# Kernel tuning notes

Hardware: AMD Instinct MI355X
Metric: run time of the kernel (lower is better)

## Reference

```python
import jax, jax.numpy as jnp
import numpy as np

DT = 0.01  # integrator base timestep (init kwarg)
DT_SCALE = 1.0


def setup_inputs() -> dict:
    key = jax.random.key(0)
    kx, kv, kf, ku, kw = jax.random.split(key, 5)
    B, D, R = 8192, 1024, 256
    scale = 1.0 / np.sqrt(D)
    return {
        "x": jax.random.normal(kx, (B, D), jnp.float32),
        "v": jax.random.normal(kv, (B, D), jnp.float32),
        "force": jax.random.normal(kf, (B, D), jnp.float32) * 0.1,
        "U": jax.random.normal(ku, (R, D), jnp.float32) * scale,
        "W": jax.random.normal(kw, (R, D), jnp.float32) * scale,
        "steps": 4,
    }


def _christoffel(v, x, U, W):
    # Low-rank Christoffel contraction Gamma(v, v; x):
    #   h = tanh(x W^T)   [B, r]  (position-dependent gating)
    #   q = v W^T         [B, r]  (velocity projection)
    #   Gamma = (h * q^2) U  [B, d]
    h = jnp.tanh(x @ W.T)
    q = v @ W.T
    return (h * q * q) @ U


def reference(x, v, force, U, W, steps):
    # topology_id == 0 (Euclidean): apply_boundary is the identity.
    dt = DT * DT_SCALE

    def dynamics(cx, cv):
        return -_christoffel(cv, cx, U, W) + force

    cx, cv = x, v
    for _ in range(steps):  # steps is a static Python int
        dx1 = cv
        dv1 = dynamics(cx, cv)
        v2 = cv + 0.5 * dt * dv1
        x2 = cx + 0.5 * dt * dx1
        dx2 = v2
        dv2 = dynamics(x2, v2)
        v3 = cv + 0.5 * dt * dv2
        x3 = cx + 0.5 * dt * dx2
        dx3 = v3
        dv3 = dynamics(x3, v3)
        v4 = cv + dt * dv3
        x4 = cx + dt * dx3
        dx4 = v4
        dv4 = dynamics(x4, v4)
        cx = cx + (dt / 6.0) * (dx1 + 2 * dx2 + 2 * dx3 + dx4)
        cv = cv + (dt / 6.0) * (dv1 + 2 * dv2 + 2 * dv3 + dv4)
    return (cx, cv)
```

## Files before the change

kernel.cpp:

```cpp
#include <hip/hip_runtime.h>


typedef __attribute__((ext_vector_type(8))) short bf16x8;
typedef __attribute__((ext_vector_type(4))) float f32x4;
typedef unsigned short us;

#define MFMA16 __builtin_amdgcn_mfma_f32_16x16x32_bf16

namespace {
constexpr int kB = 8192;
constexpr int kD = 1024;
constexpr int kR = 256;
constexpr int kBM = 16;
constexpr float kDt = 0.01f;
}

__device__ __forceinline__ us f2bf(float f) {
  union { float f; unsigned u; } w; w.f = f;
  unsigned u = w.u + (0x7FFFu + ((w.u >> 16) & 1u));
  return (us)(u >> 16);
}
__device__ __forceinline__ float ftanh(float x) {
  float e = __expf(2.f * x);
  return 1.f - 2.f / (e + 1.f);
}
__device__ __forceinline__ bf16x8 pack8(float4 a, float4 b) {
  union { bf16x8 v; us s[8]; } u;
  u.s[0] = f2bf(a.x); u.s[1] = f2bf(a.y); u.s[2] = f2bf(a.z); u.s[3] = f2bf(a.w);
  u.s[4] = f2bf(b.x); u.s[5] = f2bf(b.y); u.s[6] = f2bf(b.z); u.s[7] = f2bf(b.w);
  return u.v;
}

__global__ void prep_wu(const float* __restrict__ U, const float* __restrict__ W,
                        us* __restrict__ Wb, us* __restrict__ Ub,
                        us* __restrict__ Wf, us* __restrict__ Uf) {
  int i = blockIdx.x * blockDim.x + threadIdx.x;
  if (i < kR * kD) {
    const int r = i >> 10, k = i & 1023;
    const us wb = f2bf(W[i]), ub = f2bf(U[i]);
    Wb[i] = wb; Ub[i] = ub;
    Wf[(((size_t)(r >> 4) * 32 + (k >> 5)) << 9) +
       (((((k >> 3) & 3) << 4) | (r & 15)) << 3) + (k & 7)] = wb;
    Uf[(((size_t)(k >> 4) * 8 + (r >> 5)) << 9) +
       (((((r >> 3) & 3) << 4) | (k & 15)) << 3) + (r & 7)] = ub;
  }
}

__global__ __launch_bounds__(256) void prep_g(const us* __restrict__ Wb,
                                              const us* __restrict__ Ub,
                                              us* __restrict__ Gf) {
  const int tid = threadIdx.x;
  const int w = tid >> 6, l = tid & 63;
  const int l15 = l & 15, l4 = l >> 4;
  const int n1 = (blockIdx.x >> 3) * 32 + (w >> 1) * 16;
  const int k1 = (blockIdx.x & 7) * 32 + (w & 1) * 16;
  f32x4 acc = {0.f, 0.f, 0.f, 0.f};
  const us* wp = Wb + (size_t)(n1 + l15) * kD + l4 * 8;
  const us* up = Ub + (size_t)(k1 + l15) * kD + l4 * 8;
#pragma unroll 8
  for (int kk = 0; kk < 32; ++kk) {
    bf16x8 aw = *(const bf16x8*)(wp + kk * 32);
    bf16x8 bu = *(const bf16x8*)(up + kk * 32);
    acc = MFMA16(aw, bu, acc, 0, 0, 0);
  }
#pragma unroll
  for (int j = 0; j < 4; ++j) {
    const int n = n1 + l4 * 4 + j, k = k1 + l15;
    Gf[(((size_t)(n >> 4) * 8 + (k >> 5)) << 9) +
       (((((k >> 3) & 3) << 4) | (n & 15)) << 3) + (k & 7)] = f2bf(acc[j]);
  }
}

__global__ __launch_bounds__(1024, 4) void fused_kernel(
    const us* __restrict__ Wf, const us* __restrict__ Gf, const us* __restrict__ Uf,
    const float* __restrict__ xin, const float* __restrict__ vin,
    const float* __restrict__ force,
    float* __restrict__ cxo, float* __restrict__ cvo) {
  __shared__ __align__(16) us stg[12288];
  __shared__ __align__(16) us ct[2][kBM * kR];

  const int tid = threadIdx.x;
  const int w = tid >> 6;
  const int l = tid & 63;
  const int l15 = l & 15;
  const int l4 = l >> 4;
  const int rs = l15 & 7;
  const int brow = blockIdx.x * kBM;
  const int rn = w * 16 + l15;
  const float dt = kDt;
  const f32x4 zero4 = {0.f, 0.f, 0.f, 0.f};

  const int slotA = tid & 511;
  const int rowA = slotA >> 5, grpA = slotA & 31;
  const int soA = (rowA << 8) + ((grpA ^ (rowA & 7)) << 3);
  us* dstA = stg + ((tid >> 9) << 12);
  const float* srcA = (tid >> 9) ? vin : xin;
  const size_t gbA0 = (size_t)(brow + rowA) * kD + grpA * 8;

  f32x4 Aa = zero4, Ba = zero4, Fa = zero4;
#pragma unroll 1
  for (int ch = 0; ch < 4; ++ch) {
    const size_t gb = gbA0 + (size_t)ch * 256;
    float4 a0 = *(const float4*)(srcA + gb), a1 = *(const float4*)(srcA + gb + 4);
    float4 b0, b1;
    if (tid < 512) { b0 = *(const float4*)(force + gb); b1 = *(const float4*)(force + gb + 4); }
    if (ch) __syncthreads();
    *(bf16x8*)(dstA + soA) = pack8(a0, a1);
    if (tid < 512) *(bf16x8*)(stg + 8192 + soA) = pack8(b0, b1);
    __syncthreads();

    const us* wfp = Wf + (((size_t)(w * 32 + ch * 8)) << 9) + l * 8;
    bf16x8 bw = *(const bf16x8*)(wfp);
#pragma unroll
    for (int kk = 0; kk < 8; ++kk) {
      const bf16x8 bwc = bw;
      if (kk < 7) bw = *(const bf16x8*)(wfp + (((size_t)(kk + 1)) << 9));
      const int aoff = (l15 << 8) + (((kk * 4 + l4) ^ rs) << 3);
      bf16x8 ax = *(const bf16x8*)(stg + aoff);
      bf16x8 av = *(const bf16x8*)(stg + 4096 + aoff);
      bf16x8 af = *(const bf16x8*)(stg + 8192 + aoff);
      Aa = MFMA16(ax, bwc, Aa, 0, 0, 0);
      Ba = MFMA16(av, bwc, Ba, 0, 0, 0);
      Fa = MFMA16(af, bwc, Fa, 0, 0, 0);
    }
  }

  bf16x8 gfr[8];
  {
    const us* gfp = Gf + ((size_t)(w * 8) << 9) + l * 8;
#pragma unroll
    for (int kk = 0; kk < 8; ++kk)
      gfr[kk] = *(const bf16x8*)(gfp + ((size_t)kk << 9));
  }

  float A[4], Bv[4], Fv[4], q[4], CS[4], PS[4], Sv[4], Sx[4];
#pragma unroll
  for (int e = 0; e < 4; ++e) {
    A[e] = Aa[e]; Bv[e] = Ba[e]; Fv[e] = Fa[e]; Sv[e] = 0.f; Sx[e] = 0.f;
  }

  int wo[4];
#pragma unroll
  for (int e = 0; e < 4; ++e) {
    const int r = l4 * 4 + e;
    wo[e] = (r << 8) + ((((rn >> 3) ^ (r & 7)) << 3) | (rn & 7));
  }

  __syncthreads();
#pragma unroll 1
  for (int s = 0; s < 4; ++s) {
#pragma unroll
    for (int e = 0; e < 4; ++e) { q[e] = Bv[e]; CS[e] = 0.f; PS[e] = 0.f; }

#pragma unroll
    for (int k = 0; k < 4; ++k) {
      const float alpha = (k == 0) ? 0.f : ((k == 3) ? dt : 0.5f * dt);
      const float wk = (k == 1 || k == 2) ? 2.f : 1.f;
      const float beta = (k <= 1) ? 0.5f * dt : dt;
      float c[4];
#pragma unroll
      for (int e = 0; e < 4; ++e) {
        const float hx = A[e] + alpha * Bv[e];
        c[e] = ftanh(hx) * q[e] * q[e];
        CS[e] += wk * c[e];
      }
      if (s == 3 && k == 3) break;

      us* cb = ct[k & 1];
#pragma unroll
      for (int e = 0; e < 4; ++e) cb[wo[e]] = f2bf(c[e]);
      __syncthreads();

      f32x4 P = zero4;
#pragma unroll
      for (int kk = 0; kk < 8; ++kk) {
        bf16x8 ca = *(const bf16x8*)(cb + (l15 << 8) + (((kk * 4 + l4) ^ rs) << 3));
        P = MFMA16(ca, gfr[kk], P, 0, 0, 0);
      }
#pragma unroll
      for (int e = 0; e < 4; ++e) {
        PS[e] += wk * P[e];
        if (k < 3) q[e] = Bv[e] + beta * (Fv[e] - P[e]);
      }
    }

#pragma unroll
    for (int e = 0; e < 4; ++e) Sv[e] += CS[e];
    if (s < 3) {
      const float wsx = (float)(3 - s);
#pragma unroll
      for (int e = 0; e < 4; ++e) {
        Sx[e] += wsx * CS[e];
        A[e] += dt * Bv[e];
        Bv[e] += dt * Fv[e] - (dt / 6.f) * PS[e];
      }
    }
  }

  __syncthreads();
#pragma unroll
  for (int e = 0; e < 4; ++e) {
    ct[0][wo[e]] = f2bf(Sv[e]);
    ct[1][wo[e]] = f2bf(Sx[e]);
  }
  __syncthreads();

#pragma unroll 1
  for (int nt = 0; nt < 4; ++nt) {
    f32x4 gv = zero4, gx = zero4;
    const int d0 = w * 64 + nt * 16;
    const us* ufp = Uf + ((size_t)((w * 4 + nt) * 8) << 9) + l * 8;
#pragma unroll
    for (int kk = 0; kk < 8; ++kk) {
      const int aoff = (l15 << 8) + (((kk * 4 + l4) ^ rs) << 3);
      bf16x8 ub = *(const bf16x8*)(ufp + ((size_t)kk << 9));
      gv = MFMA16(*(const bf16x8*)(ct[0] + aoff), ub, gv, 0, 0, 0);
      gx = MFMA16(*(const bf16x8*)(ct[1] + aoff), ub, gx, 0, 0, 0);
    }
#pragma unroll
    for (int j = 0; j < 4; ++j) {
      const int row = l4 * 4 + j;
      const size_t gi = (size_t)(brow + row) * kD + d0 + l15;
      const float x0 = xin[gi], v0 = vin[gi], f = force[gi];
      cxo[gi] = x0 + 4.f * dt * v0 + 6.f * dt * dt * f - (dt * dt / 6.f) * gx[j];
      cvo[gi] = v0 + 4.f * dt * f - (dt / 6.f) * gv[j];
    }
  }
}

__global__ void copy_only_kernel(const float* __restrict__ x, const float* __restrict__ v,
                                 float* __restrict__ cx, float* __restrict__ cv) {
  const int stride = gridDim.x * blockDim.x;
  for (int i = blockIdx.x * blockDim.x + threadIdx.x; i < kB * kD; i += stride) {
    cx[i] = x[i]; cv[i] = v[i];
  }
}

extern "C" void kernel_launch(void* const* d_in, const int* in_sizes, int n_in,
                              void* d_out, int out_size, void* d_ws, size_t ws_size,
                              hipStream_t stream) {
  const float* x = (const float*)d_in[0];
  const float* v = (const float*)d_in[1];
  const float* force = (const float*)d_in[2];
  const float* U = (const float*)d_in[3];
  const float* W = (const float*)d_in[4];

  float* cx = (float*)d_out;
  float* cv = cx + (size_t)kB * kD;

  size_t off = 0;
  us* Wb = (us*)((char*)d_ws + off); off += (size_t)kR * kD * 2;
  us* Ub = (us*)((char*)d_ws + off); off += (size_t)kR * kD * 2;
  us* Wf = (us*)((char*)d_ws + off); off += (size_t)kR * kD * 2;
  us* Uf = (us*)((char*)d_ws + off); off += (size_t)kR * kD * 2;
  us* Gf = (us*)((char*)d_ws + off); off += (size_t)kR * kR * 2;

  if (ws_size < off) {
    copy_only_kernel<<<2048, 256, 0, stream>>>(x, v, cx, cv);
    return;
  }

  prep_wu<<<(kR * kD + 255) / 256, 256, 0, stream>>>(U, W, Wb, Ub, Wf, Uf);
  prep_g<<<64, 256, 0, stream>>>(Wb, Ub, Gf);
  fused_kernel<<<kB / kBM, 1024, 0, stream>>>(Wf, Gf, Uf, x, v, force, cx, cv);
}
```

Measured before the change: 117.5 us.

## Double-buffer input staging and prefetch next chunk during MFMA projection

Doubles the shared staging buffer so each of the four input chunks goes into an alternating buffer. The global loads for the next chunk are issued right after the barrier, so they overlap with the MFMA work on the current chunk, and the extra barrier before each write is removed. Every thread now loads x, v and force as float4 and packs them with the HIP bf16 intrinsics instead of hand-written rounding. The cost is a larger shared-memory footprint, which may reduce occupancy for the 1024-thread block, and one barrier before the main loop is dropped, which depends on the ct buffer not aliasing the staging area.

```diff
diff --git a/kernel.cpp b/kernel.cpp
--- a/kernel.cpp
+++ b/kernel.cpp
@@ -1,7 +1,9 @@
 #include <hip/hip_runtime.h>
+#include <hip/hip_bf16.h>
 
 
 typedef __attribute__((ext_vector_type(8))) short bf16x8;
+typedef __attribute__((ext_vector_type(4))) short bf16x4;
 typedef __attribute__((ext_vector_type(4))) float f32x4;
 typedef unsigned short us;
 
@@ -16,19 +18,19 @@
 }
 
 __device__ __forceinline__ us f2bf(float f) {
-  union { float f; unsigned u; } w; w.f = f;
-  unsigned u = w.u + (0x7FFFu + ((w.u >> 16) & 1u));
-  return (us)(u >> 16);
+  __hip_bfloat16 h = __float2bfloat16(f);
+  union { __hip_bfloat16 b; us u; } c; c.b = h;
+  return c.u;
+}
+__device__ __forceinline__ bf16x4 pack4(float4 a) {
+  union { bf16x4 v; __hip_bfloat162 h[2]; } u;
+  u.h[0] = __float22bfloat162_rn(float2{a.x, a.y});
+  u.h[1] = __float22bfloat162_rn(float2{a.z, a.w});
+  return u.v;
 }
 __device__ __forceinline__ float ftanh(float x) {
   float e = __expf(2.f * x);
   return 1.f - 2.f / (e + 1.f);
-}
-__device__ __forceinline__ bf16x8 pack8(float4 a, float4 b) {
-  union { bf16x8 v; us s[8]; } u;
-  u.s[0] = f2bf(a.x); u.s[1] = f2bf(a.y); u.s[2] = f2bf(a.z); u.s[3] = f2bf(a.w);
-  u.s[4] = f2bf(b.x); u.s[5] = f2bf(b.y); u.s[6] = f2bf(b.z); u.s[7] = f2bf(b.w);
-  return u.v;
 }
 
 __global__ void prep_wu(const float* __restrict__ U, const float* __restrict__ W,
@@ -76,7 +78,7 @@
     const float* __restrict__ xin, const float* __restrict__ vin,
     const float* __restrict__ force,
     float* __restrict__ cxo, float* __restrict__ cvo) {
-  __shared__ __align__(16) us stg[12288];
+  __shared__ __align__(16) us stg[24576];
   __shared__ __align__(16) us ct[2][kBM * kR];
 
   const int tid = threadIdx.x;
@@ -90,38 +92,43 @@
   const float dt = kDt;
   const f32x4 zero4 = {0.f, 0.f, 0.f, 0.f};
 
-  const int slotA = tid & 511;
-  const int rowA = slotA >> 5, grpA = slotA & 31;
-  const int soA = (rowA << 8) + ((grpA ^ (rowA & 7)) << 3);
-  us* dstA = stg + ((tid >> 9) << 12);
-  const float* srcA = (tid >> 9) ? vin : xin;
-  const size_t gbA0 = (size_t)(brow + rowA) * kD + grpA * 8;
+  const int prow = tid >> 6;
+  const int pg = (tid & 63) >> 1;
+  const int pso = (prow << 8) + ((pg ^ (prow & 7)) << 3) + (tid & 1) * 4;
+  const size_t pgb0 = (size_t)(brow + prow) * kD + (tid & 63) * 4;
 
   f32x4 Aa = zero4, Ba = zero4, Fa = zero4;
+  {
+    float4 xr = *(const float4*)(xin + pgb0);
+    float4 vr = *(const float4*)(vin + pgb0);
+    float4 fr = *(const float4*)(force + pgb0);
 #pragma unroll 1
-  for (int ch = 0; ch < 4; ++ch) {
-    const size_t gb = gbA0 + (size_t)ch * 256;
-    float4 a0 = *(const float4*)(srcA + gb), a1 = *(const float4*)(srcA + gb + 4);
-    float4 b0, b1;
-    if (tid < 512) { b0 = *(const float4*)(force + gb); b1 = *(const float4*)(force + gb + 4); }
-    if (ch) __syncthreads();
-    *(bf16x8*)(dstA + soA) = pack8(a0, a1);
-    if (tid < 512) *(bf16x8*)(stg + 8192 + soA) = pack8(b0, b1);
-    __syncthreads();
-
-    const us* wfp = Wf + (((size_t)(w * 32 + ch * 8)) << 9) + l * 8;
-    bf16x8 bw = *(const bf16x8*)(wfp);
-#pragma unroll
-    for (int kk = 0; kk < 8; ++kk) {
-      const bf16x8 bwc = bw;
-      if (kk < 7) bw = *(const bf16x8*)(wfp + (((size_t)(kk + 1)) << 9));
-      const int aoff = (l15 << 8) + (((kk * 4 + l4) ^ rs) << 3);
-      bf16x8 ax = *(const bf16x8*)(stg + aoff);
-      bf16x8 av = *(const bf16x8*)(stg + 4096 + aoff);
-      bf16x8 af = *(const bf16x8*)(stg + 8192 + aoff);
-      Aa = MFMA16(ax, bwc, Aa, 0, 0, 0);
-      Ba = MFMA16(av, bwc, Ba, 0, 0, 0);
-      Fa = MFMA16(af, bwc, Fa, 0, 0, 0);
+    for (int ch = 0; ch < 4; ++ch) {
+      us* sb = stg + (ch & 1) * 12288;
+      *(bf16x4*)(sb + pso) = pack4(xr);
+      *(bf16x4*)(sb + 4096 + pso) = pack4(vr);
+      *(bf16x4*)(sb + 8192 + pso) = pack4(fr);
+      __syncthreads();
+      if (ch < 3) {
+        const size_t gb = pgb0 + (size_t)(ch + 1) * 256;
+        xr = *(const float4*)(xin + gb);
+        vr = *(const float4*)(vin + gb);
+        fr = *(const float4*)(force + gb);
+      }
+      const us* wfp = Wf + (((size_t)(w * 32 + ch * 8)) << 9) + l * 8;
+      bf16x8 bw = *(const bf16x8*)(wfp);
+#pragma unroll
+      for (int kk = 0; kk < 8; ++kk) {
+        const bf16x8 bwc = bw;
+        if (kk < 7) bw = *(const bf16x8*)(wfp + (((size_t)(kk + 1)) << 9));
+        const int aoff = (l15 << 8) + (((kk * 4 + l4) ^ rs) << 3);
+        bf16x8 ax = *(const bf16x8*)(sb + aoff);
+        bf16x8 av = *(const bf16x8*)(sb + 4096 + aoff);
+        bf16x8 af = *(const bf16x8*)(sb + 8192 + aoff);
+        Aa = MFMA16(ax, bwc, Aa, 0, 0, 0);
+        Ba = MFMA16(av, bwc, Ba, 0, 0, 0);
+        Fa = MFMA16(af, bwc, Fa, 0, 0, 0);
+      }
     }
   }
 
@@ -146,7 +153,6 @@
     wo[e] = (r << 8) + ((((rn >> 3) ^ (r & 7)) << 3) | (rn & 7));
   }
 
-  __syncthreads();
 #pragma unroll 1
   for (int s = 0; s < 4; ++s) {
 #pragma unroll
```

After: 113.8 us. 3.1% less time.
